# Performance work log

Hardware: AMD Instinct MI355X
Metric: run time of the kernel (lower is better)

The kernel has to match this reference:

```python
import jax, jax.numpy as jnp
import numpy as np

B, S, D, H = 4, 1024, 1024, 16
DH = D // H  # head dim = 64
PAD = -1e7   # padding_num in source
EPS = 1e-3   # keras LayerNormalization default epsilon


def setup_inputs() -> dict:
    key = jax.random.key(0)
    ks = jax.random.split(key, 8)
    return {
        "queries": jax.random.normal(ks[0], (B, S, D), jnp.float32),
        "keys": jax.random.normal(ks[1], (B, S, D), jnp.float32),
        "values": jax.random.normal(ks[2], (B, S, D), jnp.float32),
        "query_masks": jax.random.randint(ks[3], (B, S), 0, 2, jnp.int32),
        "key_masks": jax.random.randint(ks[4], (B, S), 0, 2, jnp.int32),
        "Wq": jax.random.normal(ks[5], (D, D), jnp.float32) * (D ** -0.5),
        "Wk": jax.random.normal(ks[6], (D, D), jnp.float32) * (D ** -0.5),
        "Wv": jax.random.normal(ks[7], (D, D), jnp.float32) * (D ** -0.5),
        "gamma": jnp.ones((D,), jnp.float32),
        "beta": jnp.zeros((D,), jnp.float32),
    }


def reference(queries, keys, values, query_masks, key_masks, Wq, Wk, Wv, gamma, beta):
    # QKV projections (no bias)
    Q = queries @ Wq  # [B,S,D]
    K = keys @ Wk
    V = values @ Wv
    # split heads: tf.split(axis=2)+concat(axis=0) == head-major layout [H,B,S,DH]
    Qh = Q.reshape(B, S, H, DH).transpose(2, 0, 1, 3)
    Kh = K.reshape(B, S, H, DH).transpose(2, 0, 1, 3)
    Vh = V.reshape(B, S, H, DH).transpose(2, 0, 1, 3)
    # scaled scores; note source scales by head_dim ** 0.5 (d_k of split K)
    scores = jnp.einsum("hbqd,hbkd->hbqk", Qh, Kh) / (DH ** 0.5)
    # additive key mask: positions where key_mask==0 get large negative
    scores = jnp.where(key_masks[None, :, None, :] == 0, PAD, scores)
    attn = jax.nn.softmax(scores, axis=-1)
    # multiplicative query mask AFTER softmax (as in source)
    attn = attn * query_masks[None, :, :, None].astype(jnp.float32)
    out = jnp.einsum("hbqk,hbkd->hbqd", attn, Vh)  # [H,B,S,DH]
    # merge heads back: concat over feature axis in head order
    out = out.transpose(1, 2, 0, 3).reshape(B, S, D)
    # residual + LayerNorm
    res = queries + out
    mean = jnp.mean(res, axis=-1, keepdims=True)
    var = jnp.mean(jnp.square(res - mean), axis=-1, keepdims=True)
    return gamma * (res - mean) * jax.lax.rsqrt(var + EPS) + beta
```

## Files before the change

### kernel.cpp

```cpp
#include <hip/hip_runtime.h>

#define BB   4
#define SS   1024
#define DD   1024
#define HH   16
#define DHH  64
#define LN_EPS  (1e-3f)

typedef unsigned short u16;
typedef __attribute__((ext_vector_type(8))) short bf16x8;
typedef __attribute__((ext_vector_type(4))) float f32x4;

__device__ __forceinline__ u16 f2bf(float f) {
    union { float f; unsigned int u; } v; v.f = f;
    return (u16)((v.u + 0x7FFFu + ((v.u >> 16) & 1u)) >> 16);
}

__device__ __forceinline__ unsigned int cvt_pk_bf16(float lo, float hi) {
    unsigned int r;
    asm("v_cvt_pk_bf16_f32 %0, %1, %2" : "=v"(r) : "v"(lo), "v"(hi));
    return r;
}

__device__ __forceinline__ void cp16(void* lds, const void* g) {
    __builtin_amdgcn_global_load_lds(
        (const __attribute__((address_space(1))) unsigned int*)g,
        (__attribute__((address_space(3))) unsigned int*)lds, 16, 0, 0);
}

__global__ __launch_bounds__(256) void prep(const float* __restrict__ q,
                                            const float* __restrict__ k,
                                            const float* __restrict__ v,
                                            const float* __restrict__ Wq,
                                            const float* __restrict__ Wk,
                                            const float* __restrict__ Wv,
                                            u16* __restrict__ Abf,
                                            u16* __restrict__ WtA) {
    __shared__ float Ts[64][65];
    const int z = blockIdx.z;
    const int tid = threadIdx.x;
    if (z < 3) {
        const float* src = (z == 0) ? q : (z == 1) ? k : v;
        u16* dst = Abf + (size_t)z * ((size_t)BB * SS * DD);
        const int N8 = BB * SS * DD / 8;
        for (int i = blockIdx.x * 256 + tid; i < N8; i += 256 * 256) {
            const float4 f0 = ((const float4*)src)[i * 2];
            const float4 f1 = ((const float4*)src)[i * 2 + 1];
            union { u16 u[8]; uint4 o; } t;
            t.u[0] = f2bf(f0.x); t.u[1] = f2bf(f0.y);
            t.u[2] = f2bf(f0.z); t.u[3] = f2bf(f0.w);
            t.u[4] = f2bf(f1.x); t.u[5] = f2bf(f1.y);
            t.u[6] = f2bf(f1.z); t.u[7] = f2bf(f1.w);
            ((uint4*)dst)[i] = t.o;
        }
    } else {
        const float* W = (z == 3) ? Wq : (z == 4) ? Wk : Wv;
        u16* Wt = WtA + (size_t)(z - 3) * DD * DD;
        const int k0 = (blockIdx.x >> 4) * 64, n0 = (blockIdx.x & 15) * 64;
        #pragma unroll
        for (int it = 0; it < 4; ++it) {
            const int idx = tid + it * 256;
            const int r = idx >> 4, c4 = (idx & 15) * 4;
            const float4 vv = *(const float4*)&W[(size_t)(k0 + r) * DD + n0 + c4];
            Ts[r][c4 + 0] = vv.x; Ts[r][c4 + 1] = vv.y;
            Ts[r][c4 + 2] = vv.z; Ts[r][c4 + 3] = vv.w;
        }
        __syncthreads();
        const int n = tid >> 2, kc = (tid & 3) * 16;
        #pragma unroll
        for (int p = 0; p < 8; ++p) {
            const unsigned int lo = f2bf(Ts[kc + p * 2 + 0][n]);
            const unsigned int hi = f2bf(Ts[kc + p * 2 + 1][n]);
            *(unsigned int*)&Wt[(size_t)(n0 + n) * DD + k0 + kc + p * 2] = lo | (hi << 16);
        }
    }
}

__global__ __launch_bounds__(256, 3) void gemm_fused(const u16* __restrict__ Abf,
                                                     const u16* __restrict__ WtA,
                                                     u16* __restrict__ Qbf,
                                                     u16* __restrict__ Kbf,
                                                     u16* __restrict__ Vtb) {
    __shared__ u16 As[128 * 64];
    __shared__ u16 Bs[128 * 64];

    const int bid = blockIdx.x;
    const int swz = (bid & 7) * 96 + (bid >> 3);
    const int z   = swz >> 8;
    const int rem = swz & 255;
    const int m0  = (rem >> 3) * 128;
    const int n0  = (rem & 7) * 128;

    const u16* A  = Abf + (size_t)z * ((size_t)BB * SS * DD);
    const u16* Bm = WtA + (size_t)z * (DD * DD);

    const int tid  = threadIdx.x;
    const int wave = tid >> 6, lane = tid & 63;
    const int ln = lane & 15, quad = lane >> 4;
    const int mw = (wave & 1) * 64, nw = (wave >> 1) * 64;

    const int r0 = tid >> 3;
    const int c0 = (tid & 7) ^ (r0 & 7);
    const u16* srcA0 = A  + (size_t)(m0 + r0) * DD + c0 * 8;
    const u16* srcB0 = Bm + (size_t)(n0 + r0) * DD + c0 * 8;

    f32x4 acc[4][4] = {};

    for (int t = 0; t < 16; ++t) {
        const int koff = t * 64;
        __syncthreads();
        #pragma unroll
        for (int w = 0; w < 4; ++w) {
            cp16(&As[(w * 256 + wave * 64) * 8], srcA0 + (size_t)w * 32 * DD + koff);
            cp16(&Bs[(w * 256 + wave * 64) * 8], srcB0 + (size_t)w * 32 * DD + koff);
        }
        __syncthreads();

        #pragma unroll
        for (int kk = 0; kk < 2; ++kk) {
            bf16x8 af[4], bfv[4];
            #pragma unroll
            for (int i = 0; i < 4; ++i) {
                const int r = mw + i * 16 + ln;
                af[i] = *(const bf16x8*)&As[((r << 3) + ((kk * 4 + quad) ^ (r & 7))) << 3];
            }
            #pragma unroll
            for (int j = 0; j < 4; ++j) {
                const int r = nw + j * 16 + ln;
                bfv[j] = *(const bf16x8*)&Bs[((r << 3) + ((kk * 4 + quad) ^ (r & 7))) << 3];
            }
            __builtin_amdgcn_s_setprio(1);
            #pragma unroll
            for (int i = 0; i < 4; ++i)
                #pragma unroll
                for (int j = 0; j < 4; ++j)
                    acc[i][j] = __builtin_amdgcn_mfma_f32_16x16x32_bf16(af[i], bfv[j], acc[i][j], 0, 0, 0);
            __builtin_amdgcn_s_setprio(0);
        }
    }

    if (z < 2) {
        u16* C = (z == 0) ? Qbf : Kbf;
        const float scale = (z == 0) ? 0.18033688f : 1.0f;
        #pragma unroll
        for (int i = 0; i < 4; ++i) {
            const int mbase = m0 + mw + i * 16 + quad * 4;
            const int bb = mbase >> 10, sb = mbase & 1023;
            #pragma unroll
            for (int j = 0; j < 4; ++j) {
                const int n = n0 + nw + j * 16 + ln;
                const int hh = n >> 6, dh = n & 63;
                #pragma unroll
                for (int r = 0; r < 4; ++r)
                    C[(((size_t)bb * HH + hh) * SS + sb + r) * DHH + dh] =
                        f2bf(acc[i][j][r] * scale);
            }
        }
    } else {
        #pragma unroll
        for (int i = 0; i < 4; ++i) {
            const int mbase = m0 + mw + i * 16 + quad * 4;
            const int bb = mbase >> 10, sb = mbase & 1023;
            #pragma unroll
            for (int j = 0; j < 4; ++j) {
                const int n = n0 + nw + j * 16 + ln;
                const int hh = n >> 6, dh = n & 63;
                uint2 pk;
                pk.x = cvt_pk_bf16(acc[i][j][0], acc[i][j][1]);
                pk.y = cvt_pk_bf16(acc[i][j][2], acc[i][j][3]);
                *(uint2*)&Vtb[(((size_t)bb * HH + hh) * DHH + dh) * SS + sb] = pk;
            }
        }
    }
}

__global__ __launch_bounds__(512) void attn_mfma(const u16* __restrict__ Qg,
                                                 const u16* __restrict__ Kg,
                                                 const u16* __restrict__ Vtg,
                                                 const int* __restrict__ qmask,
                                                 const int* __restrict__ kmask,
                                                 float* __restrict__ O) {
    __shared__ u16 Ps[128 * 68];
    __shared__ u16 Ks[2][64 * 64];
    __shared__ u16 Vs[2][64 * 64];
    __shared__ float kmLds[SS];

    const int bid  = blockIdx.x;
    const int xcd  = bid & 7;
    const int rest = bid >> 3;
    const int bh   = (rest & 7) * 8 + xcd;
    const int qt   = rest >> 3;
    const int b    = bh >> 4, h = bh & 15;
    const int q0   = qt * 128;
    const int tid  = threadIdx.x;
    const int wave = tid >> 6, lane = tid & 63;
    const int ln = lane & 15, quad = lane >> 4;
    const size_t bhs = (size_t)b * HH + h;

    const int sr = tid >> 3, scsrc = (tid & 7) ^ ((tid >> 3) & 7);
    const u16* kSrc = &Kg[(bhs * SS + sr) * DHH + scsrc * 8];
    const u16* vSrc = &Vtg[(bhs * DHH + sr) * SS + scsrc * 8];
    auto stageKV = [&](int t) {
        const int cb = t & 1;
        cp16(&Ks[cb][wave * 512], kSrc + (size_t)t * 64 * DHH);
        cp16(&Vs[cb][wave * 512], vSrc + t * 64);
    };

    const u16* qrow = &Qg[(bhs * SS + q0 + wave * 16 + ln) * DHH];
    const bf16x8 qf0 = *(const bf16x8*)&qrow[quad * 8];
    const bf16x8 qf1 = *(const bf16x8*)&qrow[32 + quad * 8];
    asm volatile("" ::: "memory");
    if (wave < 4)
        cp16(&kmLds[wave * 256], &kmask[b * SS + (wave * 64 + lane) * 4]);
    stageKV(0);
    stageKV(1);
    asm volatile("s_waitcnt vmcnt(2)" ::: "memory");
    __builtin_amdgcn_s_barrier();

    {
        const int2 iv = *(const int2*)&kmLds[tid * 2];
        float2 fv; fv.x = (float)iv.x; fv.y = (float)iv.y;
        *(float2*)&kmLds[tid * 2] = fv;
    }
    asm volatile("s_waitcnt lgkmcnt(0)" ::: "memory");
    __builtin_amdgcn_s_barrier();

    int off[4][2];
    #pragma unroll
    for (int nt = 0; nt < 4; ++nt) {
        const int r = nt * 16 + ln;
        off[nt][0] = ((r << 3) + ((0 + quad) ^ (r & 7))) << 3;
        off[nt][1] = ((r << 3) + ((4 + quad) ^ (r & 7))) << 3;
    }

    f32x4 o[4] = {};
    float lsum = 0.f;
    const f32x4 zero = {0.f, 0.f, 0.f, 0.f};
    const int prow = (wave * 16 + ln) * 68;

    #pragma unroll 2
    for (int kt = 0; kt < SS / 64; ++kt) {
        const int cb = kt & 1;
        const u16* Kc = Ks[cb];
        const u16* Vc = Vs[cb];

        #pragma unroll
        for (int nt = 0; nt < 4; ++nt) {
            const bf16x8 k0f = *(const bf16x8*)&Kc[off[nt][0]];
            const bf16x8 k1f = *(const bf16x8*)&Kc[off[nt][1]];
            f32x4 sacc = __builtin_amdgcn_mfma_f32_16x16x32_bf16(k0f, qf0, zero, 0, 0, 0);
            sacc = __builtin_amdgcn_mfma_f32_16x16x32_bf16(k1f, qf1, sacc, 0, 0, 0);
            const float4 fm = *(const float4*)&kmLds[kt * 64 + nt * 16 + quad * 4];
            const float p0 = fm.x * __builtin_amdgcn_exp2f(sacc[0]);
            const float p1 = fm.y * __builtin_amdgcn_exp2f(sacc[1]);
            const float p2 = fm.z * __builtin_amdgcn_exp2f(sacc[2]);
            const float p3 = fm.w * __builtin_amdgcn_exp2f(sacc[3]);
            lsum += (p0 + p1) + (p2 + p3);
            uint2 pk;
            pk.x = cvt_pk_bf16(p0, p1);
            pk.y = cvt_pk_bf16(p2, p3);
            *(uint2*)&Ps[prow + nt * 16 + quad * 4] = pk;
        }

        __builtin_amdgcn_s_setprio(1);
        #pragma unroll
        for (int kk2 = 0; kk2 < 2; ++kk2) {
            const bf16x8 pf = *(const bf16x8*)&Ps[prow + kk2 * 32 + quad * 8];
            #pragma unroll
            for (int nt2 = 0; nt2 < 4; ++nt2) {
                const bf16x8 vf = *(const bf16x8*)&Vc[off[nt2][kk2]];
                o[nt2] = __builtin_amdgcn_mfma_f32_16x16x32_bf16(pf, vf, o[nt2], 0, 0, 0);
            }
        }
        __builtin_amdgcn_s_setprio(0);

        if (kt == SS / 64 - 1) break;
        __builtin_amdgcn_s_barrier();
        if (kt + 2 < SS / 64) {
            stageKV(kt + 2);
            asm volatile("s_waitcnt vmcnt(2)" ::: "memory");
        } else {
            asm volatile("s_waitcnt vmcnt(0)" ::: "memory");
        }
        __builtin_amdgcn_s_barrier();
    }

    lsum += __shfl_xor(lsum, 16);
    lsum += __shfl_xor(lsum, 32);
    #pragma unroll
    for (int r = 0; r < 4; ++r) {
        const int qloc = quad * 4 + r;
        const float l = __shfl(lsum, qloc);
        const int q = q0 + wave * 16 + qloc;
        const float scale = (float)qmask[b * SS + q] / l;
        #pragma unroll
        for (int nt2 = 0; nt2 < 4; ++nt2)
            O[((size_t)b * SS + q) * DD + h * DHH + nt2 * 16 + ln] = o[nt2][r] * scale;
    }
}

__global__ __launch_bounds__(256) void ln_kernel(const float* __restrict__ Qin,
                                                 const float* __restrict__ attn,
                                                 const float* __restrict__ gamma,
                                                 const float* __restrict__ beta,
                                                 float* __restrict__ out) {
    const int row = blockIdx.x;
    const int tid = threadIdx.x;
    const int wid = tid >> 6, lane = tid & 63;
    __shared__ float sred[4];

    const float4 qv = ((const float4*)Qin)[(size_t)row * 256 + tid];
    const float4 av = ((const float4*)attn)[(size_t)row * 256 + tid];
    float4 v;
    v.x = qv.x + av.x; v.y = qv.y + av.y;
    v.z = qv.z + av.z; v.w = qv.w + av.w;

    float sum = v.x + v.y + v.z + v.w;
    #pragma unroll
    for (int off = 32; off; off >>= 1) sum += __shfl_down(sum, off);
    if (lane == 0) sred[wid] = sum;
    __syncthreads();
    const float mean = (sred[0] + sred[1] + sred[2] + sred[3]) * (1.0f / DD);
    __syncthreads();

    const float dx = v.x - mean, dy = v.y - mean, dz = v.z - mean, dw = v.w - mean;
    float vs = dx * dx + dy * dy + dz * dz + dw * dw;
    #pragma unroll
    for (int off = 32; off; off >>= 1) vs += __shfl_down(vs, off);
    if (lane == 0) sred[wid] = vs;
    __syncthreads();
    const float var = (sred[0] + sred[1] + sred[2] + sred[3]) * (1.0f / DD);
    const float inv = rsqrtf(var + LN_EPS);

    const float4 g = ((const float4*)gamma)[tid];
    const float4 bt = ((const float4*)beta)[tid];
    float4 ov;
    ov.x = g.x * dx * inv + bt.x; ov.y = g.y * dy * inv + bt.y;
    ov.z = g.z * dz * inv + bt.z; ov.w = g.w * dw * inv + bt.w;
    ((float4*)out)[(size_t)row * 256 + tid] = ov;
}

extern "C" void kernel_launch(void* const* d_in, const int* in_sizes, int n_in,
                              void* d_out, int out_size, void* d_ws, size_t ws_size,
                              hipStream_t stream) {
    const float* queries = (const float*)d_in[0];
    const float* keys    = (const float*)d_in[1];
    const float* values  = (const float*)d_in[2];
    const int*   qmask   = (const int*)d_in[3];
    const int*   kmask   = (const int*)d_in[4];
    const float* Wq      = (const float*)d_in[5];
    const float* Wk      = (const float*)d_in[6];
    const float* Wv      = (const float*)d_in[7];
    const float* gamma   = (const float*)d_in[8];
    const float* beta    = (const float*)d_in[9];
    float* out = (float*)d_out;

    const size_t NTOK = (size_t)BB * SS;
    u16* Abf = (u16*)d_ws;
    float* Ob = (float*)d_ws;
    u16* Qbf = Abf + 3 * NTOK * DD;
    u16* Kbf = Qbf + NTOK * DD;
    u16* Vtb = Kbf + NTOK * DD;
    u16* WtA = Vtb + NTOK * DD;

    prep<<<dim3(256, 1, 6), 256, 0, stream>>>(queries, keys, values, Wq, Wk, Wv, Abf, WtA);

    gemm_fused<<<768, 256, 0, stream>>>(Abf, WtA, Qbf, Kbf, Vtb);

    attn_mfma<<<BB * HH * (SS / 128), 512, 0, stream>>>(Qbf, Kbf, Vtb, qmask, kmask, Ob);

    ln_kernel<<<BB * SS, 256, 0, stream>>>(queries, Ob, gamma, beta, out);
}
```

Baseline: 179.1 us.

## Halve attention block threads, each wave processes two 16-row query tiles

The attention kernel now launches 256 threads (4 waves) per block instead of 512, and each wave handles 32 query rows as two 16-row sub-tiles. Each K/V fragment read from LDS is reused across both sub-tiles, and K/V staging is split into two copy rounds per thread. The aim is less LDS read traffic per MFMA and fewer waves taking part in block barriers. In exchange each wave holds more accumulator registers, and there are fewer resident waves to hide latency.

```diff
diff --git a/kernel.cpp b/kernel.cpp
--- a/kernel.cpp
+++ b/kernel.cpp
@@ -174,7 +174,7 @@
     }
 }
 
-__global__ __launch_bounds__(512) void attn_mfma(const u16* __restrict__ Qg,
+__global__ __launch_bounds__(256) void attn_mfma(const u16* __restrict__ Qg,
                                                  const u16* __restrict__ Kg,
                                                  const u16* __restrict__ Vtg,
                                                  const int* __restrict__ qmask,
@@ -197,30 +197,38 @@
     const int ln = lane & 15, quad = lane >> 4;
     const size_t bhs = (size_t)b * HH + h;
 
-    const int sr = tid >> 3, scsrc = (tid & 7) ^ ((tid >> 3) & 7);
-    const u16* kSrc = &Kg[(bhs * SS + sr) * DHH + scsrc * 8];
-    const u16* vSrc = &Vtg[(bhs * DHH + sr) * SS + scsrc * 8];
+    const int sr  = tid >> 3;
+    const int scs = (tid & 7) ^ (sr & 7);
+    const u16* kS = &Kg[(bhs * SS + sr) * DHH + scs * 8];
+    const u16* vS = &Vtg[(bhs * DHH + sr) * SS + scs * 8];
     auto stageKV = [&](int t) {
         const int cb = t & 1;
-        cp16(&Ks[cb][wave * 512], kSrc + (size_t)t * 64 * DHH);
-        cp16(&Vs[cb][wave * 512], vSrc + t * 64);
+        #pragma unroll
+        for (int rd = 0; rd < 2; ++rd) {
+            cp16(&Ks[cb][(rd * 256 + wave * 64) * 8], kS + ((size_t)t * 64 + rd * 32) * DHH);
+            cp16(&Vs[cb][(rd * 256 + wave * 64) * 8], vS + (size_t)rd * 32 * SS + t * 64);
+        }
     };
 
-    const u16* qrow = &Qg[(bhs * SS + q0 + wave * 16 + ln) * DHH];
-    const bf16x8 qf0 = *(const bf16x8*)&qrow[quad * 8];
-    const bf16x8 qf1 = *(const bf16x8*)&qrow[32 + quad * 8];
+    const u16* qbase = &Qg[(bhs * SS + q0 + wave * 32 + ln) * DHH];
+    bf16x8 qf[2][2];
+    qf[0][0] = *(const bf16x8*)&qbase[quad * 8];
+    qf[0][1] = *(const bf16x8*)&qbase[32 + quad * 8];
+    qf[1][0] = *(const bf16x8*)&qbase[16 * DHH + quad * 8];
+    qf[1][1] = *(const bf16x8*)&qbase[16 * DHH + 32 + quad * 8];
     asm volatile("" ::: "memory");
-    if (wave < 4)
-        cp16(&kmLds[wave * 256], &kmask[b * SS + (wave * 64 + lane) * 4]);
+    cp16(&kmLds[wave * 256], &kmask[b * SS + tid * 4]);
     stageKV(0);
     stageKV(1);
-    asm volatile("s_waitcnt vmcnt(2)" ::: "memory");
+    asm volatile("s_waitcnt vmcnt(4)" ::: "memory");
     __builtin_amdgcn_s_barrier();
 
     {
-        const int2 iv = *(const int2*)&kmLds[tid * 2];
-        float2 fv; fv.x = (float)iv.x; fv.y = (float)iv.y;
-        *(float2*)&kmLds[tid * 2] = fv;
+        const int4 iv = *(const int4*)&kmLds[tid * 4];
+        float4 fv;
+        fv.x = (float)iv.x; fv.y = (float)iv.y;
+        fv.z = (float)iv.z; fv.w = (float)iv.w;
+        *(float4*)&kmLds[tid * 4] = fv;
     }
     asm volatile("s_waitcnt lgkmcnt(0)" ::: "memory");
     __builtin_amdgcn_s_barrier();
@@ -233,10 +241,11 @@
         off[nt][1] = ((r << 3) + ((4 + quad) ^ (r & 7))) << 3;
     }
 
-    f32x4 o[4] = {};
-    float lsum = 0.f;
+    f32x4 o[2][4] = {};
+    float lsum[2] = {0.f, 0.f};
     const f32x4 zero = {0.f, 0.f, 0.f, 0.f};
-    const int prow = (wave * 16 + ln) * 68;
+    const int prow0 = (wave * 32 + ln) * 68;
+    const int prow1 = (wave * 32 + 16 + ln) * 68;
 
     #pragma unroll 2
     for (int kt = 0; kt < SS / 64; ++kt) {
@@ -245,31 +254,39 @@
         const u16* Vc = Vs[cb];
 
         #pragma unroll
-        for (int nt = 0; nt < 4; ++nt) {
-            const bf16x8 k0f = *(const bf16x8*)&Kc[off[nt][0]];
-            const bf16x8 k1f = *(const bf16x8*)&Kc[off[nt][1]];
-            f32x4 sacc = __builtin_amdgcn_mfma_f32_16x16x32_bf16(k0f, qf0, zero, 0, 0, 0);
-            sacc = __builtin_amdgcn_mfma_f32_16x16x32_bf16(k1f, qf1, sacc, 0, 0, 0);
-            const float4 fm = *(const float4*)&kmLds[kt * 64 + nt * 16 + quad * 4];
-            const float p0 = fm.x * __builtin_amdgcn_exp2f(sacc[0]);
-            const float p1 = fm.y * __builtin_amdgcn_exp2f(sacc[1]);
-            const float p2 = fm.z * __builtin_amdgcn_exp2f(sacc[2]);
-            const float p3 = fm.w * __builtin_amdgcn_exp2f(sacc[3]);
-            lsum += (p0 + p1) + (p2 + p3);
-            uint2 pk;
-            pk.x = cvt_pk_bf16(p0, p1);
-            pk.y = cvt_pk_bf16(p2, p3);
-            *(uint2*)&Ps[prow + nt * 16 + quad * 4] = pk;
+        for (int qs = 0; qs < 2; ++qs) {
+            const int prow = qs ? prow1 : prow0;
+            #pragma unroll
+            for (int nt = 0; nt < 4; ++nt) {
+                const bf16x8 k0f = *(const bf16x8*)&Kc[off[nt][0]];
+                const bf16x8 k1f = *(const bf16x8*)&Kc[off[nt][1]];
+                f32x4 sacc = __builtin_amdgcn_mfma_f32_16x16x32_bf16(k0f, qf[qs][0], zero, 0, 0, 0);
+                sacc = __builtin_amdgcn_mfma_f32_16x16x32_bf16(k1f, qf[qs][1], sacc, 0, 0, 0);
+                const float4 fm = *(const float4*)&kmLds[kt * 64 + nt * 16 + quad * 4];
+                const float p0 = fm.x * __builtin_amdgcn_exp2f(sacc[0]);
+                const float p1 = fm.y * __builtin_amdgcn_exp2f(sacc[1]);
+                const float p2 = fm.z * __builtin_amdgcn_exp2f(sacc[2]);
+                const float p3 = fm.w * __builtin_amdgcn_exp2f(sacc[3]);
+                lsum[qs] += (p0 + p1) + (p2 + p3);
+                uint2 pk;
+                pk.x = cvt_pk_bf16(p0, p1);
+                pk.y = cvt_pk_bf16(p2, p3);
+                *(uint2*)&Ps[prow + nt * 16 + quad * 4] = pk;
+            }
         }
 
         __builtin_amdgcn_s_setprio(1);
         #pragma unroll
-        for (int kk2 = 0; kk2 < 2; ++kk2) {
-            const bf16x8 pf = *(const bf16x8*)&Ps[prow + kk2 * 32 + quad * 8];
-            #pragma unroll
-            for (int nt2 = 0; nt2 < 4; ++nt2) {
-                const bf16x8 vf = *(const bf16x8*)&Vc[off[nt2][kk2]];
-                o[nt2] = __builtin_amdgcn_mfma_f32_16x16x32_bf16(pf, vf, o[nt2], 0, 0, 0);
+        for (int qs = 0; qs < 2; ++qs) {
+            const int prow = qs ? prow1 : prow0;
+            #pragma unroll
+            for (int kk2 = 0; kk2 < 2; ++kk2) {
+                const bf16x8 pf = *(const bf16x8*)&Ps[prow + kk2 * 32 + quad * 8];
+                #pragma unroll
+                for (int nt2 = 0; nt2 < 4; ++nt2) {
+                    const bf16x8 vf = *(const bf16x8*)&Vc[off[nt2][kk2]];
+                    o[qs][nt2] = __builtin_amdgcn_mfma_f32_16x16x32_bf16(pf, vf, o[qs][nt2], 0, 0, 0);
+                }
             }
         }
         __builtin_amdgcn_s_setprio(0);
@@ -278,24 +295,27 @@
         __builtin_amdgcn_s_barrier();
         if (kt + 2 < SS / 64) {
             stageKV(kt + 2);
-            asm volatile("s_waitcnt vmcnt(2)" ::: "memory");
+            asm volatile("s_waitcnt vmcnt(4)" ::: "memory");
         } else {
             asm volatile("s_waitcnt vmcnt(0)" ::: "memory");
         }
         __builtin_amdgcn_s_barrier();
     }
 
-    lsum += __shfl_xor(lsum, 16);
-    lsum += __shfl_xor(lsum, 32);
     #pragma unroll
-    for (int r = 0; r < 4; ++r) {
-        const int qloc = quad * 4 + r;
-        const float l = __shfl(lsum, qloc);
-        const int q = q0 + wave * 16 + qloc;
-        const float scale = (float)qmask[b * SS + q] / l;
-        #pragma unroll
-        for (int nt2 = 0; nt2 < 4; ++nt2)
-            O[((size_t)b * SS + q) * DD + h * DHH + nt2 * 16 + ln] = o[nt2][r] * scale;
+    for (int qs = 0; qs < 2; ++qs) {
+        lsum[qs] += __shfl_xor(lsum[qs], 16);
+        lsum[qs] += __shfl_xor(lsum[qs], 32);
+        #pragma unroll
+        for (int r = 0; r < 4; ++r) {
+            const int qloc = quad * 4 + r;
+            const float l = __shfl(lsum[qs], qloc);
+            const int q = q0 + wave * 32 + qs * 16 + qloc;
+            const float scale = (float)qmask[b * SS + q] / l;
+            #pragma unroll
+            for (int nt2 = 0; nt2 < 4; ++nt2)
+                O[((size_t)b * SS + q) * DD + h * DHH + nt2 * 16 + ln] = o[qs][nt2][r] * scale;
+        }
     }
 }
 
@@ -367,7 +387,7 @@
 
     gemm_fused<<<768, 256, 0, stream>>>(Abf, WtA, Qbf, Kbf, Vtb);
 
-    attn_mfma<<<BB * HH * (SS / 128), 512, 0, stream>>>(Qbf, Kbf, Vtb, qmask, kmask, Ob);
+    attn_mfma<<<BB * HH * (SS / 128), 256, 0, stream>>>(Qbf, Kbf, Vtb, qmask, kmask, Ob);
 
     ln_kernel<<<BB * SS, 256, 0, stream>>>(queries, Ob, gamma, beta, out);
 }
```

Measured after the change: 193.0 us. 7.8% more time.

## Triple-buffer K/V tiles with one barrier per step; wave-per-row LayerNorm

Applied to the files above, without the earlier changes.

The attention loop moves from double to triple buffering of K/V tiles in LDS. The next-next tile is issued at the top of each iteration, so each step needs one barrier instead of two. Separately, LayerNorm now gives each row to one wave and reduces with xor shuffles, removing LDS reductions and __syncthreads and launching a quarter as many blocks. Both changes use more LDS or registers per block, which could reduce occupancy.

```diff
diff --git a/kernel.cpp b/kernel.cpp
--- a/kernel.cpp
+++ b/kernel.cpp
@@ -181,8 +181,8 @@
                                                  const int* __restrict__ kmask,
                                                  float* __restrict__ O) {
     __shared__ u16 Ps[128 * 68];
-    __shared__ u16 Ks[2][64 * 64];
-    __shared__ u16 Vs[2][64 * 64];
+    __shared__ u16 Ks[3][64 * 64];
+    __shared__ u16 Vs[3][64 * 64];
     __shared__ float kmLds[SS];
 
     const int bid  = blockIdx.x;
@@ -200,8 +200,7 @@
     const int sr = tid >> 3, scsrc = (tid & 7) ^ ((tid >> 3) & 7);
     const u16* kSrc = &Kg[(bhs * SS + sr) * DHH + scsrc * 8];
     const u16* vSrc = &Vtg[(bhs * DHH + sr) * SS + scsrc * 8];
-    auto stageKV = [&](int t) {
-        const int cb = t & 1;
+    auto stageKV = [&](int cb, int t) {
         cp16(&Ks[cb][wave * 512], kSrc + (size_t)t * 64 * DHH);
         cp16(&Vs[cb][wave * 512], vSrc + t * 64);
     };
@@ -212,8 +211,8 @@
     asm volatile("" ::: "memory");
     if (wave < 4)
         cp16(&kmLds[wave * 256], &kmask[b * SS + (wave * 64 + lane) * 4]);
-    stageKV(0);
-    stageKV(1);
+    stageKV(0, 0);
+    stageKV(1, 1);
     asm volatile("s_waitcnt vmcnt(2)" ::: "memory");
     __builtin_amdgcn_s_barrier();
 
@@ -238,11 +237,12 @@
     const f32x4 zero = {0.f, 0.f, 0.f, 0.f};
     const int prow = (wave * 16 + ln) * 68;
 
-    #pragma unroll 2
+    int cbC = 0, cbS = 2;
     for (int kt = 0; kt < SS / 64; ++kt) {
-        const int cb = kt & 1;
-        const u16* Kc = Ks[cb];
-        const u16* Vc = Vs[cb];
+        if (kt + 2 < SS / 64) stageKV(cbS, kt + 2);
+
+        const u16* Kc = Ks[cbC];
+        const u16* Vc = Vs[cbC];
 
         #pragma unroll
         for (int nt = 0; nt < 4; ++nt) {
@@ -274,15 +274,13 @@
         }
         __builtin_amdgcn_s_setprio(0);
 
-        if (kt == SS / 64 - 1) break;
-        __builtin_amdgcn_s_barrier();
-        if (kt + 2 < SS / 64) {
-            stageKV(kt + 2);
-            asm volatile("s_waitcnt vmcnt(2)" ::: "memory");
-        } else {
-            asm volatile("s_waitcnt vmcnt(0)" ::: "memory");
-        }
-        __builtin_amdgcn_s_barrier();
+        if (kt < SS / 64 - 1) {
+            if (kt + 2 < SS / 64) asm volatile("s_waitcnt vmcnt(2)" ::: "memory");
+            else                  asm volatile("s_waitcnt vmcnt(0)" ::: "memory");
+            __builtin_amdgcn_s_barrier();
+        }
+        cbC = (cbC == 2) ? 0 : cbC + 1;
+        cbS = (cbS == 2) ? 0 : cbS + 1;
     }
 
     lsum += __shfl_xor(lsum, 16);
@@ -304,40 +302,50 @@
                                                  const float* __restrict__ gamma,
                                                  const float* __restrict__ beta,
                                                  float* __restrict__ out) {
-    const int row = blockIdx.x;
     const int tid = threadIdx.x;
     const int wid = tid >> 6, lane = tid & 63;
-    __shared__ float sred[4];
-
-    const float4 qv = ((const float4*)Qin)[(size_t)row * 256 + tid];
-    const float4 av = ((const float4*)attn)[(size_t)row * 256 + tid];
-    float4 v;
-    v.x = qv.x + av.x; v.y = qv.y + av.y;
-    v.z = qv.z + av.z; v.w = qv.w + av.w;
-
-    float sum = v.x + v.y + v.z + v.w;
-    #pragma unroll
-    for (int off = 32; off; off >>= 1) sum += __shfl_down(sum, off);
-    if (lane == 0) sred[wid] = sum;
-    __syncthreads();
-    const float mean = (sred[0] + sred[1] + sred[2] + sred[3]) * (1.0f / DD);
-    __syncthreads();
-
-    const float dx = v.x - mean, dy = v.y - mean, dz = v.z - mean, dw = v.w - mean;
-    float vs = dx * dx + dy * dy + dz * dz + dw * dw;
-    #pragma unroll
-    for (int off = 32; off; off >>= 1) vs += __shfl_down(vs, off);
-    if (lane == 0) sred[wid] = vs;
-    __syncthreads();
-    const float var = (sred[0] + sred[1] + sred[2] + sred[3]) * (1.0f / DD);
-    const float inv = rsqrtf(var + LN_EPS);
-
-    const float4 g = ((const float4*)gamma)[tid];
-    const float4 bt = ((const float4*)beta)[tid];
-    float4 ov;
-    ov.x = g.x * dx * inv + bt.x; ov.y = g.y * dy * inv + bt.y;
-    ov.z = g.z * dz * inv + bt.z; ov.w = g.w * dw * inv + bt.w;
-    ((float4*)out)[(size_t)row * 256 + tid] = ov;
+    const int row = blockIdx.x * 4 + wid;
+    const float4* qp = (const float4*)Qin + (size_t)row * 256;
+    const float4* ap = (const float4*)attn + (size_t)row * 256;
+
+    float4 v[4];
+    float sum = 0.f;
+    #pragma unroll
+    for (int i = 0; i < 4; ++i) {
+        const float4 qv = qp[lane + 64 * i];
+        const float4 av = ap[lane + 64 * i];
+        float4 t;
+        t.x = qv.x + av.x; t.y = qv.y + av.y;
+        t.z = qv.z + av.z; t.w = qv.w + av.w;
+        v[i] = t;
+        sum += (t.x + t.y) + (t.z + t.w);
+    }
+    #pragma unroll
+    for (int off = 1; off < 64; off <<= 1) sum += __shfl_xor(sum, off);
+    const float mean = sum * (1.0f / DD);
+
+    float vs = 0.f;
+    #pragma unroll
+    for (int i = 0; i < 4; ++i) {
+        const float dx = v[i].x - mean, dy = v[i].y - mean;
+        const float dz = v[i].z - mean, dw = v[i].w - mean;
+        vs += (dx * dx + dy * dy) + (dz * dz + dw * dw);
+    }
+    #pragma unroll
+    for (int off = 1; off < 64; off <<= 1) vs += __shfl_xor(vs, off);
+    const float inv = rsqrtf(vs * (1.0f / DD) + LN_EPS);
+
+    #pragma unroll
+    for (int i = 0; i < 4; ++i) {
+        const float4 g  = ((const float4*)gamma)[lane + 64 * i];
+        const float4 bt = ((const float4*)beta)[lane + 64 * i];
+        float4 ov;
+        ov.x = g.x * (v[i].x - mean) * inv + bt.x;
+        ov.y = g.y * (v[i].y - mean) * inv + bt.y;
+        ov.z = g.z * (v[i].z - mean) * inv + bt.z;
+        ov.w = g.w * (v[i].w - mean) * inv + bt.w;
+        ((float4*)out)[(size_t)row * 256 + lane + 64 * i] = ov;
+    }
 }
 
 extern "C" void kernel_launch(void* const* d_in, const int* in_sizes, int n_in,
@@ -369,5 +377,5 @@
 
     attn_mfma<<<BB * HH * (SS / 128), 512, 0, stream>>>(Qbf, Kbf, Vtb, qmask, kmask, Ob);
 
-    ln_kernel<<<BB * SS, 256, 0, stream>>>(queries, Ob, gamma, beta, out);
-}
+    ln_kernel<<<BB * SS / 4, 256, 0, stream>>>(queries, Ob, gamma, beta, out);
+}
```

Result: no change. 182.7 us (+2.0%).
